# Performance work log

Measured on AMD Instinct MI355X. Metric: run time of the kernel, lower is better.

Reference implementation:

```python
import jax, jax.numpy as jnp
import numpy as np

B, T_PAST, T_FUT, GH, GW = 256, 20, 30, 100, 100
HID = 32  # past_encoder_dim


def gru_cell(x, h, w_ih, w_hh, b_ih, b_hh):
    # torch nn.GRU single-cell math; weights [3H, in], [3H, H]
    gi = x @ w_ih.T + b_ih
    gh = h @ w_hh.T + b_hh
    i_r, i_z, i_n = jnp.split(gi, 3, axis=-1)
    h_r, h_z, h_n = jnp.split(gh, 3, axis=-1)
    r = jax.nn.sigmoid(i_r + h_r)
    zg = jax.nn.sigmoid(i_z + h_z)
    n = jnp.tanh(i_n + r * h_n)
    return (1.0 - zg) * n + zg * h


def bilinear(grid, q):
    # grid [B,H,W,C]; q [B,2], dim 0 -> height, dim 1 -> width (matches torch code)
    Bn, Hh, Ww, C = grid.shape
    fy = jnp.clip(jnp.floor(q[:, 0]), 0.0, Hh - 2).astype(jnp.int32)
    fx = jnp.clip(jnp.floor(q[:, 1]), 0.0, Ww - 2).astype(jnp.int32)
    ay = jnp.clip(q[:, 0] - fy, 0.0, 1.0)[:, None]
    ax = jnp.clip(q[:, 1] - fx, 0.0, 1.0)[:, None]
    b = jnp.arange(Bn)
    tl = grid[b, fy, fx]
    tr = grid[b, fy, fx + 1]
    bl = grid[b, fy + 1, fx]
    br = grid[b, fy + 1, fx + 1]
    top = tl + ax * (tr - tl)
    bot = bl + ax * (br - bl)
    return top + ay * (bot - top)  # [B,C]


def setup_inputs() -> dict:
    key = jax.random.key(0)
    ks = jax.random.split(key, 24)
    s = 0.05
    f32 = jnp.float32
    inp = {
        'z': jax.random.normal(ks[0], (B, T_FUT, 2), f32),
        'player_past': jax.random.uniform(ks[1], (B, T_PAST, 2), f32) * (GH - 10),
        'lidar': jax.random.normal(ks[2], (B, GH, GW, 2), f32),
        'conv0_w': jax.random.normal(ks[3], (2, 2, 2, 32), f32) * s,   # HWIO
        'conv0_b': jnp.zeros((32,), f32),
        'conv1_w': jax.random.normal(ks[4], (2, 2, 32, 32), f32) * s,
        'conv1_b': jnp.zeros((32,), f32),
        'conv2_w': jax.random.normal(ks[5], (2, 2, 32, 32), f32) * s,
        'conv2_b': jnp.zeros((32,), f32),
        'conv3_w': jax.random.normal(ks[6], (2, 2, 32, 32), f32) * s,
        'conv3_b': jnp.zeros((32,), f32),
        'enc_wih': jax.random.normal(ks[7], (3 * HID, 2), f32) * s,
        'enc_whh': jax.random.normal(ks[8], (3 * HID, HID), f32) * s,
        'enc_bih': jnp.zeros((3 * HID,), f32),
        'enc_bhh': jnp.zeros((3 * HID,), f32),
        'dec_wih': jax.random.normal(ks[9], (3 * HID, HID + 2), f32) * s,
        'dec_whh': jax.random.normal(ks[10], (3 * HID, HID), f32) * s,
        'dec_bih': jnp.zeros((3 * HID,), f32),
        'dec_bhh': jnp.zeros((3 * HID,), f32),
        'mlp_w1': jax.random.normal(ks[11], (512, HID), f32) * s,
        'mlp_b1': jnp.zeros((512,), f32),
        'mlp_w2': jax.random.normal(ks[12], (4, 512), f32) * s,
        'mlp_b2': jnp.zeros((4,), f32),
    }
    return inp


def reference(z, player_past, lidar,
              conv0_w, conv0_b, conv1_w, conv1_b, conv2_w, conv2_b, conv3_w, conv3_b,
              enc_wih, enc_whh, enc_bih, enc_bhh,
              dec_wih, dec_whh, dec_bih, dec_bhh,
              mlp_w1, mlp_b1, mlp_w2, mlp_b2):
    # field model: ZeroPad2d((0,1,0,1)) + Conv 2x2 + ReLU, x4 -> same-size NHWC conv
    v = lidar
    for w, b in ((conv0_w, conv0_b), (conv1_w, conv1_b), (conv2_w, conv2_b), (conv3_w, conv3_b)):
        v = jax.nn.relu(jax.lax.conv_general_dilated(
            v, w, (1, 1), [(0, 1), (0, 1)],
            dimension_numbers=('NHWC', 'HWIO', 'NHWC')) + b)
    context_lidar = v  # [B,GH,GW,32]

    # past encoder GRU; last output of single-layer GRU == final hidden
    h0 = jnp.zeros((z.shape[0], HID), z.dtype)
    def enc_step(h, x_t):
        return gru_cell(x_t, h, enc_wih, enc_whh, enc_bih, enc_bhh), None
    h_enc, _ = jax.lax.scan(enc_step, h0, jnp.swapaxes(player_past, 0, 1))

    y_tm2 = player_past[:, -2, :]
    y_tm1 = player_past[:, -1, :]

    def dec_step(carry, z_t):
        h, y1, y2 = carry
        interp_t = bilinear(context_lidar, y1)                 # [B,32]
        x = jnp.concatenate([y1, interp_t], axis=-1)            # [B,34]
        h = gru_cell(x, h, dec_wih, dec_whh, dec_bih, dec_bhh)
        # locscale_mlp: Linear(32,512) -> Linear(512,4) (no ReLU between, per source)
        ls = (h @ mlp_w1.T + mlp_b1) @ mlp_w2.T + mlp_b2
        loc = ls[:, :2]
        scale = jax.nn.softplus(ls[:, 2:])
        y_t = 2.0 * y1 - y2 + loc + scale * z_t                 # verlet + affine sample
        return (h, y_t, y1), (y_t, scale)

    _, (ys, scales) = jax.lax.scan(dec_step, (h_enc, y_tm1, y_tm2), jnp.swapaxes(z, 0, 1))
    y = jnp.swapaxes(ys, 0, 1)          # [B,T,2]
    scales = jnp.swapaxes(scales, 0, 1)  # [B,T,2]
    logabsdet = jnp.sum(jnp.log(jnp.abs(jnp.prod(scales, axis=-2))), axis=-1)  # [B]
    return (y, logabsdet)
```

## Files before the change

kernel.cpp:

```cpp
#include <hip/hip_runtime.h>
#include <math.h>

typedef __attribute__((ext_vector_type(8))) short    short8;
typedef __attribute__((ext_vector_type(4))) float    f32x4;
typedef __attribute__((ext_vector_type(4))) unsigned uint4v;

#define FRAG0 256

__device__ __forceinline__ unsigned short f2bf(float f) {
    unsigned u = __builtin_bit_cast(unsigned, f);
    u = u + 0x7fffu + ((u >> 16) & 1u);
    return (unsigned short)(u >> 16);
}
__device__ __forceinline__ unsigned packRNE(float hi, float lo) {
    return (unsigned)f2bf(lo) | ((unsigned)f2bf(hi) << 16);
}
__device__ __forceinline__ unsigned pack_trunc(float hi, float lo) {
    return __builtin_amdgcn_perm(__builtin_bit_cast(unsigned, hi),
                                 __builtin_bit_cast(unsigned, lo), 0x07060302u);
}
__device__ __forceinline__ float rfl(float x) {
    return __builtin_bit_cast(float, __builtin_amdgcn_readfirstlane(__builtin_bit_cast(int, x)));
}
__device__ __forceinline__ f32x4 mfma16(short8 a, short8 b, f32x4 c) {
    return __builtin_amdgcn_mfma_f32_16x16x32_bf16(a, b, c, 0, 0, 0);
}
__device__ __forceinline__ unsigned bperm(int addr, unsigned v) {
    return (unsigned)__builtin_amdgcn_ds_bpermute(addr, (int)v);
}
template<int PAT>
__device__ __forceinline__ float swzXf(float v) {
    return __builtin_bit_cast(float, __builtin_amdgcn_ds_swizzle(__builtin_bit_cast(int, v), PAT));
}
__device__ __forceinline__ unsigned swz1u(unsigned v){ return (unsigned)__builtin_amdgcn_ds_swizzle((int)v, 0x041F); }
__device__ __forceinline__ float sigf(float x) { return __builtin_amdgcn_rcpf(1.f + __expf(-x)); }
__device__ __forceinline__ float tanhfast(float x) {
    float e = __expf(2.f * x);
    return 1.f - 2.f * __builtin_amdgcn_rcpf(e + 1.f);
}
__device__ __forceinline__ f32x4 ld4(const float* p) { return *(const f32x4*)p; }

__device__ __forceinline__ void packC(unsigned* P, f32x4 a0, f32x4 a1, bool oob) {
    float r0 = fmaxf(a0[0], 0.f), r1 = fmaxf(a0[1], 0.f), r2 = fmaxf(a0[2], 0.f), r3 = fmaxf(a0[3], 0.f);
    float s0 = fmaxf(a1[0], 0.f), s1 = fmaxf(a1[1], 0.f), s2 = fmaxf(a1[2], 0.f), s3 = fmaxf(a1[3], 0.f);
    P[0] = pack_trunc(r1, r0); P[1] = pack_trunc(r3, r2);
    P[2] = pack_trunc(s1, s0); P[3] = pack_trunc(s3, s2);
    if (oob) { P[0] = 0u; P[1] = 0u; P[2] = 0u; P[3] = 0u; }
}

__global__ __launch_bounds__(256) void r2p2_prep(
    const float* __restrict__ w0, const float* __restrict__ w1,
    const float* __restrict__ w2, const float* __restrict__ w3,
    const float* __restrict__ enc_whh,
    const float* __restrict__ dec_wih, const float* __restrict__ dec_whh,
    const float* __restrict__ mw1, const float* __restrict__ mb1,
    const float* __restrict__ mw2, const float* __restrict__ mb2,
    float* __restrict__ wsf, unsigned* __restrict__ wsu) {
    const int tid = threadIdx.x, bx = blockIdx.x;
    __shared__ __align__(16) short s[4224];
    __shared__ float red[64];

    if (bx == 0) {
        if (tid < 128) {
            int k = tid & 31, j = tid >> 5;
            const float* w2r = mw2 + j * 512;
            float a0 = 0.f, a1 = 0.f, a2 = 0.f, a3 = 0.f;
#pragma unroll 4
            for (int m = 0; m < 512; m += 4) {
                a0 = fmaf(w2r[m],     mw1[m * 32 + k],       a0);
                a1 = fmaf(w2r[m + 1], mw1[(m + 1) * 32 + k], a1);
                a2 = fmaf(w2r[m + 2], mw1[(m + 2) * 32 + k], a2);
                a3 = fmaf(w2r[m + 3], mw1[(m + 3) * 32 + k], a3);
            }
            wsf[j * 32 + k] = (a0 + a1) + (a2 + a3);
        } else if (tid < 192) {
            int t = tid - 128;
            int j = t & 3, ch = t >> 2;
            const float* w2c = mw2 + j * 512 + ch * 32;
            const float* b1c = mb1 + ch * 32;
            float p = 0.f;
#pragma unroll 8
            for (int m = 0; m < 32; ++m) p = fmaf(w2c[m], b1c[m], p);
            red[t] = p;
        }
        __syncthreads();
        if (tid < 4) {
            float c = mb2[tid];
#pragma unroll
            for (int i = 0; i < 16; ++i) c += red[tid + i * 4];
            wsf[128 + tid] = c;
        }
        return;
    }

    if (bx == 7) {
        if (tid < 64) {
            int lane = tid, n = lane & 15, q = lane >> 4;
            int pc0 = ((n >> 2) << 3) | (n & 3);
#pragma unroll
            for (int mt = 0; mt < 2; ++mt) {
                int co = pc0 + mt * 4;
                uint4v u = (uint4v)0u;
                if (q == 0) {
#pragma unroll
                    for (int i = 0; i < 4; ++i)
                        u[i] = packRNE(w0[(2 * i + 1) * 32 + co], w0[2 * i * 32 + co]);
                }
                *(uint4v*)(wsu + FRAG0 + mt * 256 + lane * 4) = u;
            }
        }
        return;
    }

    if (bx <= 3) {
        const float* W = (bx == 1) ? w1 : (bx == 2) ? w2 : w3;
        int fbase = 2 + (bx - 1) * 8;
        for (int i = tid; i < 4096; i += 256) {
            int k = i >> 5, co = i & 31;
            s[k * 33 + co] = (short)f2bf(W[i]);
        }
        __syncthreads();
        if (tid < 64) {
            int lane = tid, n = lane & 15, q = lane >> 4;
            int pc0 = ((n >> 2) << 3) | (n & 3);
#pragma unroll
            for (int mt = 0; mt < 2; ++mt) {
                int co = pc0 + mt * 4;
#pragma unroll
                for (int ks = 0; ks < 4; ++ks) {
                    uint4v u;
#pragma unroll
                    for (int i2 = 0; i2 < 4; ++i2) {
                        int k0 = ks * 32 + q * 8 + 2 * i2;
                        unsigned lo = (unsigned short)s[k0 * 33 + co];
                        unsigned hi = (unsigned short)s[(k0 + 1) * 33 + co];
                        u[i2] = lo | (hi << 16);
                    }
                    *(uint4v*)(wsu + FRAG0 + (fbase + mt * 4 + ks) * 256 + lane * 4) = u;
                }
            }
        }
        return;
    }

    {
        int fbase = (bx == 4) ? 26 : (bx == 5) ? 32 : 38;
        for (int i = tid; i < 3072; i += 256) {
            int o = i >> 5, k = i & 31;
            float v = (bx == 4) ? dec_wih[o * 34 + 2 + k] : (bx == 5) ? dec_whh[i] : enc_whh[i];
            s[o * 33 + k] = (short)f2bf(v);
        }
        __syncthreads();
        if (tid < 64) {
            int lane = tid, n = lane & 15, q = lane >> 4;
            int pc0 = ((n >> 2) << 3) | (n & 3);
#pragma unroll
            for (int g = 0; g < 3; ++g) {
#pragma unroll
                for (int mt = 0; mt < 2; ++mt) {
                    int row = g * 32 + pc0 + mt * 4;
                    uint4v u;
#pragma unroll
                    for (int i2 = 0; i2 < 4; ++i2) {
                        int k0 = q * 8 + 2 * i2;
                        unsigned lo = (unsigned short)s[row * 33 + k0];
                        unsigned hi = (unsigned short)s[row * 33 + k0 + 1];
                        u[i2] = lo | (hi << 16);
                    }
                    *(uint4v*)(wsu + FRAG0 + (fbase + g * 2 + mt) * 256 + lane * 4) = u;
                }
            }
        }
        return;
    }
}

__global__ __launch_bounds__(256)
void r2p2_main(
    const float* __restrict__ z, const float* __restrict__ past, const float* __restrict__ lidar,
    const float* __restrict__ b0, const float* __restrict__ b1,
    const float* __restrict__ b2, const float* __restrict__ b3,
    const float* __restrict__ enc_wih, const float* __restrict__ enc_bih, const float* __restrict__ enc_bhh,
    const float* __restrict__ dec_wih, const float* __restrict__ dec_bih, const float* __restrict__ dec_bhh,
    const float* __restrict__ wsf, const unsigned* __restrict__ wsu,
    float* __restrict__ out) {

    const int tid = threadIdx.x, b = blockIdx.x;
    const int wid = tid >> 6, lane = tid & 63;
    const int n = lane & 15, q = lane >> 4, e = n & 1;

    __shared__ __align__(16) unsigned sLID[104 * 104];
    __shared__ __align__(16) float PASTs[40];
    __shared__ __align__(16) float ZVs[64];

    if (wid != 0) {
        int st = tid - 64;
        if (st < 60) ZVs[st] = z[b * 60 + st];
        for (int i = st; i < 816; i += 192) {
            int idx = (i < 416) ? (10400 + i) : ((((i - 416) >> 2) * 104) + 100 + ((i - 416) & 3));
            sLID[idx] = 0u;
        }
        const float4* lp4 = (const float4*)(lidar + (size_t)b * 20000);
#pragma unroll 4
        for (int i = st; i < 5000; i += 192) {
            int r = (int)(((unsigned)i * 5243u) >> 18);
            int c2 = i - r * 50;
            float4 v = lp4[i];
            int o = r * 104 + 2 * c2;
            sLID[o]     = pack_trunc(v.y, v.x);
            sLID[o + 1] = pack_trunc(v.w, v.z);
        }
        __syncthreads();
        return;
    }

    uint4v FR[44];
#pragma unroll
    for (int f = 0; f < 44; ++f) FR[f] = *(const uint4v*)(wsu + FRAG0 + f * 256 + lane * 4);
#define FRG(f) __builtin_bit_cast(short8, FR[f])

    f32x4 cb0[2], cb1[2], cb2[2], cb3[2], gbR[2], gbZ[2], gbNi[2], gbNh[2];
    f32x4 egR[2], egZ[2], egNh[2];
#pragma unroll
    for (int mt = 0; mt < 2; ++mt) {
        int o = q * 8 + mt * 4;
        cb0[mt] = ld4(b0 + o); cb1[mt] = ld4(b1 + o); cb2[mt] = ld4(b2 + o); cb3[mt] = ld4(b3 + o);
        gbR[mt]  = ld4(dec_bih + o)      + ld4(dec_bhh + o);
        gbZ[mt]  = ld4(dec_bih + 32 + o) + ld4(dec_bhh + 32 + o);
        gbNi[mt] = ld4(dec_bih + 64 + o);
        gbNh[mt] = ld4(dec_bhh + 64 + o);
        egR[mt]  = ld4(enc_bih + o)      + ld4(enc_bhh + o);
        egZ[mt]  = ld4(enc_bih + 32 + o) + ld4(enc_bhh + 32 + o);
        egNh[mt] = ld4(enc_bhh + 64 + o);
    }
    f32x4 ebni = ld4(enc_bih + 64 + q * 8 + e * 4);
    float2 wxr[4], wxz[4], wxn[4], wexr[4], wexz[4], wexn[4];
#pragma unroll
    for (int r = 0; r < 4; ++r) {
        int c = q * 8 + e * 4 + r;
        wxr[r]  = *(const float2*)(dec_wih + c * 34);
        wxz[r]  = *(const float2*)(dec_wih + (32 + c) * 34);
        wxn[r]  = *(const float2*)(dec_wih + (64 + c) * 34);
        wexr[r] = *(const float2*)(enc_wih + c * 2);
        wexz[r] = *(const float2*)(enc_wih + (32 + c) * 2);
        wexn[r] = *(const float2*)(enc_wih + (64 + c) * 2);
    }
    short8 Am = (short8)0;
    if (n < 4) {
#pragma unroll
        for (int j = 0; j < 8; ++j) Am[j] = (short)f2bf(wsf[n * 32 + q * 8 + j]);
    }
    f32x4 mcv = {0.f, 0.f, 0.f, 0.f};
    if (q == 0) mcv = *(const f32x4*)(wsf + 128);

    if (lane < 20) *(float2*)&PASTs[2 * lane] = *(const float2*)(past + b * 40 + 2 * lane);
    float q0 = past[b * 40 + 38], q1 = past[b * 40 + 39];
    float p0 = past[b * 40 + 36], p1 = past[b * 40 + 37];
    asm volatile("s_waitcnt lgkmcnt(0)" ::: "memory");

    float hq[4] = {0.f, 0.f, 0.f, 0.f};
    short8 hfr = (short8)0;
#pragma unroll 1
    for (int t = 0; t < 20; ++t) {
        float2 xp = *(const float2*)&PASTs[2 * t];
        f32x4 gr0 = mfma16(FRG(38), hfr, egR[0]),  gr1 = mfma16(FRG(39), hfr, egR[1]);
        f32x4 gz0 = mfma16(FRG(40), hfr, egZ[0]),  gz1 = mfma16(FRG(41), hfr, egZ[1]);
        f32x4 gh0 = mfma16(FRG(42), hfr, egNh[0]), gh1 = mfma16(FRG(43), hfr, egNh[1]);
        f32x4 grS = e ? gr1 : gr0, gzS = e ? gz1 : gz0, ghS = e ? gh1 : gh0;
        float hn[4];
#pragma unroll
        for (int r = 0; r < 4; ++r) {
            float rp = grS[r] + xp.x * wexr[r].x + xp.y * wexr[r].y;
            float zp = gzS[r] + xp.x * wexz[r].x + xp.y * wexz[r].y;
            float pi = ebni[r] + xp.x * wexn[r].x + xp.y * wexn[r].y;
            float rr = sigf(rp), zz = sigf(zp);
            float tn = tanhfast(fmaf(rr, ghS[r], pi));
            float hv = tn + zz * (hq[r] - tn);
            hq[r] = hv; hn[r] = hv;
        }
        unsigned hu0 = packRNE(hn[1], hn[0]), hu1 = packRNE(hn[3], hn[2]);
        unsigned po0 = swz1u(hu0), po1 = swz1u(hu1);
        uint4v hv4;
        hv4[0] = e ? po0 : hu0; hv4[1] = e ? po1 : hu1;
        hv4[2] = e ? hu0 : po0; hv4[3] = e ? hu1 : po1;
        hfr = __builtin_bit_cast(short8, hv4);
    }

    __syncthreads();

    int py0a = n / 5, px0a = n % 5;
    int pe0b = (16 + n < 25) ? 16 + n : 24;
    int py0b = pe0b / 5, px0b = pe0b - py0b * 5;
    int ofs0a[4], ofs0b[4];
#pragma unroll
    for (int tp = 0; tp < 4; ++tp) {
        ofs0a[tp] = (py0a + (tp >> 1)) * 104 + px0a + (tp & 1);
        ofs0b[tp] = (py0b + (tp >> 1)) * 104 + px0b + (tp & 1);
    }
    int py1 = n >> 2, px1 = n & 3;
    int adr1[4], sel1m[4];
#pragma unroll
    for (int ks = 0; ks < 4; ++ks) {
        int p = (py1 + (ks >> 1)) * 5 + px1 + (ks & 1);
        adr1[ks] = (q * 16 + (p & 15)) * 4;
        sel1m[ks] = (p >= 16);
    }
    int pe2 = (n < 9) ? n : 8, py2 = pe2 / 3, px2 = pe2 - py2 * 3;
    int adr2[4];
#pragma unroll
    for (int ks = 0; ks < 4; ++ks) adr2[ks] = (q * 16 + (py2 + (ks >> 1)) * 4 + px2 + (ks & 1)) * 4;
    int pe3 = n & 3, py3 = pe3 >> 1, px3 = pe3 & 1;
    int adr3[4];
#pragma unroll
    for (int ks = 0; ks < 4; ++ks) adr3[ks] = (q * 16 + (py3 + (ks >> 1)) * 3 + px3 + (ks & 1)) * 4;
    const f32x4 zf4 = {0.f, 0.f, 0.f, 0.f};
    float la = 0.f;

#pragma unroll 1
    for (int t = 0; t < 30; ++t) {
        float2 zv = *(const float2*)&ZVs[2 * t];
        float f0 = fminf(fmaxf(floorf(q0), 0.f), 98.f);
        float f1v = fminf(fmaxf(floorf(q1), 0.f), 98.f);
        int fy = (int)f0, fx = (int)f1v;
        float ay = fminf(fmaxf(q0 - f0, 0.f), 1.f);
        float ax = fminf(fmaxf(q1 - f1v, 0.f), 1.f);
        int base = fy * 104 + fx;
        int limy = 100 - fy, limx = 100 - fx;

        short8 bfa = (short8)0, bfb = (short8)0;
        if (q == 0) {
            uint4v ua, ub;
#pragma unroll
            for (int tp = 0; tp < 4; ++tp) { ua[tp] = sLID[base + ofs0a[tp]]; ub[tp] = sLID[base + ofs0b[tp]]; }
            bfa = __builtin_bit_cast(short8, ua);
            bfb = __builtin_bit_cast(short8, ub);
        }
        f32x4 ca0 = mfma16(FRG(0), bfa, cb0[0]);
        f32x4 ca1 = mfma16(FRG(1), bfa, cb0[1]);
        f32x4 cB0 = mfma16(FRG(0), bfb, cb0[0]);
        f32x4 cB1 = mfma16(FRG(1), bfb, cb0[1]);
        unsigned Pa[4], Pb[4];
        packC(Pa, ca0, ca1, (py0a >= limy) || (px0a >= limx));
        packC(Pb, cB0, cB1, (py0b >= limy) || (px0b >= limx));

        short8 bf1[4];
#pragma unroll
        for (int ks = 0; ks < 4; ++ks) {
            uint4v bu;
#pragma unroll
            for (int u = 0; u < 4; ++u) {
                unsigned va = bperm(adr1[ks], Pa[u]);
                unsigned vb = bperm(adr1[ks], Pb[u]);
                bu[u] = sel1m[ks] ? vb : va;
            }
            bf1[ks] = __builtin_bit_cast(short8, bu);
        }
        {
            f32x4 aA = mfma16(FRG(2), bf1[0], cb1[0]); aA = mfma16(FRG(3), bf1[1], aA);
            f32x4 aB = mfma16(FRG(4), bf1[2], zf4);    aB = mfma16(FRG(5), bf1[3], aB);
            f32x4 bA = mfma16(FRG(6), bf1[0], cb1[1]); bA = mfma16(FRG(7), bf1[1], bA);
            f32x4 bB = mfma16(FRG(8), bf1[2], zf4);    bB = mfma16(FRG(9), bf1[3], bB);
            f32x4 o0 = aA + aB, o1 = bA + bB;
            packC(Pa, o0, o1, (py1 >= limy) || (px1 >= limx));
        }

        short8 bf2v[4];
#pragma unroll
        for (int ks = 0; ks < 4; ++ks) {
            uint4v bu;
#pragma unroll
            for (int u = 0; u < 4; ++u) bu[u] = bperm(adr2[ks], Pa[u]);
            bf2v[ks] = __builtin_bit_cast(short8, bu);
        }
        {
            f32x4 aA = mfma16(FRG(10), bf2v[0], cb2[0]); aA = mfma16(FRG(11), bf2v[1], aA);
            f32x4 aB = mfma16(FRG(12), bf2v[2], zf4);    aB = mfma16(FRG(13), bf2v[3], aB);
            f32x4 bA = mfma16(FRG(14), bf2v[0], cb2[1]); bA = mfma16(FRG(15), bf2v[1], bA);
            f32x4 bB = mfma16(FRG(16), bf2v[2], zf4);    bB = mfma16(FRG(17), bf2v[3], bB);
            f32x4 o0 = aA + aB, o1 = bA + bB;
            packC(Pb, o0, o1, (py2 >= limy) || (px2 >= limx));
        }

        short8 bf3v[4];
#pragma unroll
        for (int ks = 0; ks < 4; ++ks) {
            uint4v bu;
#pragma unroll
            for (int u = 0; u < 4; ++u) bu[u] = bperm(adr3[ks], Pb[u]);
            bf3v[ks] = __builtin_bit_cast(short8, bu);
        }
        short8 xf;
        {
            f32x4 aA = mfma16(FRG(18), bf3v[0], cb3[0]); aA = mfma16(FRG(19), bf3v[1], aA);
            f32x4 aB = mfma16(FRG(20), bf3v[2], zf4);    aB = mfma16(FRG(21), bf3v[3], aB);
            f32x4 bA = mfma16(FRG(22), bf3v[0], cb3[1]); bA = mfma16(FRG(23), bf3v[1], bA);
            f32x4 bB = mfma16(FRG(24), bf3v[2], zf4);    bB = mfma16(FRG(25), bf3v[3], bB);
            f32x4 o0 = aA + aB, o1 = bA + bB;
            float wy = (n & 2) ? ay : 1.f - ay;
            float wx = (n & 1) ? ax : 1.f - ax;
            float w = wy * wx;
            float t0[4], t1[4];
#pragma unroll
            for (int r = 0; r < 4; ++r) { t0[r] = fmaxf(o0[r], 0.f) * w; t1[r] = fmaxf(o1[r], 0.f) * w; }
#pragma unroll
            for (int r = 0; r < 4; ++r) {
                float a1 = swzXf<0x041F>(t0[r]), a2 = swzXf<0x081F>(t0[r]), a3 = swzXf<0x0C1F>(t0[r]);
                t0[r] = (t0[r] + a1) + (a2 + a3);
                float b1v = swzXf<0x041F>(t1[r]), b2v = swzXf<0x081F>(t1[r]), b3v = swzXf<0x0C1F>(t1[r]);
                t1[r] = (t1[r] + b1v) + (b2v + b3v);
            }
            uint4v xu;
            xu[0] = packRNE(t0[1], t0[0]); xu[1] = packRNE(t0[3], t0[2]);
            xu[2] = packRNE(t1[1], t1[0]); xu[3] = packRNE(t1[3], t1[2]);
            xf = __builtin_bit_cast(short8, xu);
        }

        f32x4 gr0 = mfma16(FRG(26), xf, gbR[0]); gr0 = mfma16(FRG(32), hfr, gr0);
        f32x4 gr1 = mfma16(FRG(27), xf, gbR[1]); gr1 = mfma16(FRG(33), hfr, gr1);
        f32x4 gz0 = mfma16(FRG(28), xf, gbZ[0]); gz0 = mfma16(FRG(34), hfr, gz0);
        f32x4 gz1 = mfma16(FRG(29), xf, gbZ[1]); gz1 = mfma16(FRG(35), hfr, gz1);
        f32x4 gi0 = mfma16(FRG(30), xf, gbNi[0]);
        f32x4 gi1 = mfma16(FRG(31), xf, gbNi[1]);
        f32x4 gh0 = mfma16(FRG(36), hfr, gbNh[0]);
        f32x4 gh1 = mfma16(FRG(37), hfr, gbNh[1]);
        f32x4 grS = e ? gr1 : gr0, gzS = e ? gz1 : gz0, giS = e ? gi1 : gi0, ghS = e ? gh1 : gh0;
        float hn[4];
#pragma unroll
        for (int r = 0; r < 4; ++r) {
            float rp = grS[r] + q0 * wxr[r].x + q1 * wxr[r].y;
            float zp = gzS[r] + q0 * wxz[r].x + q1 * wxz[r].y;
            float pi = giS[r] + q0 * wxn[r].x + q1 * wxn[r].y;
            float rr = sigf(rp), zz = sigf(zp);
            float tn = tanhfast(fmaf(rr, ghS[r], pi));
            float hv = tn + zz * (hq[r] - tn);
            hq[r] = hv; hn[r] = hv;
        }
        unsigned hu0 = packRNE(hn[1], hn[0]), hu1 = packRNE(hn[3], hn[2]);
        unsigned po0 = swz1u(hu0), po1 = swz1u(hu1);
        uint4v hv4;
        hv4[0] = e ? po0 : hu0; hv4[1] = e ? po1 : hu1;
        hv4[2] = e ? hu0 : po0; hv4[3] = e ? hu1 : po1;
        hfr = __builtin_bit_cast(short8, hv4);

        f32x4 ls = mfma16(Am, hfr, mcv);
        float l2 = ls[2], l3 = ls[3];
        float s0 = fmaxf(l2, 0.f) + __logf(1.f + __expf(-fabsf(l2)));
        float s1 = fmaxf(l3, 0.f) + __logf(1.f + __expf(-fabsf(l3)));
        float ny0 = 2.f * q0 - p0 + ls[0] + s0 * zv.x;
        float ny1 = 2.f * q1 - p1 + ls[1] + s1 * zv.y;
        if (lane == 0) {
            float2 o2 = {ny0, ny1};
            *(float2*)(out + b * 60 + 2 * t) = o2;
        }
        la += __logf(s0 * s1);
        p0 = q0; p1 = q1;
        q0 = rfl(ny0); q1 = rfl(ny1);
    }
    if (lane == 0) out[15360 + b] = la;
#undef FRG
}

extern "C" void kernel_launch(void* const* d_in, const int* in_sizes, int n_in,
                              void* d_out, int out_size, void* d_ws, size_t ws_size,
                              hipStream_t stream) {
    const float* z    = (const float*)d_in[0];
    const float* past = (const float*)d_in[1];
    const float* lid  = (const float*)d_in[2];
    const float* c0w = (const float*)d_in[3];  const float* c0b = (const float*)d_in[4];
    const float* c1w = (const float*)d_in[5];  const float* c1b = (const float*)d_in[6];
    const float* c2w = (const float*)d_in[7];  const float* c2b = (const float*)d_in[8];
    const float* c3w = (const float*)d_in[9];  const float* c3b = (const float*)d_in[10];
    const float* ewih = (const float*)d_in[11]; const float* ewhh = (const float*)d_in[12];
    const float* ebih = (const float*)d_in[13]; const float* ebhh = (const float*)d_in[14];
    const float* dwih = (const float*)d_in[15]; const float* dwhh = (const float*)d_in[16];
    const float* dbih = (const float*)d_in[17]; const float* dbhh = (const float*)d_in[18];
    const float* mw1 = (const float*)d_in[19]; const float* mb1 = (const float*)d_in[20];
    const float* mw2 = (const float*)d_in[21]; const float* mb2 = (const float*)d_in[22];
    float* out = (float*)d_out;
    float* wsf = (float*)d_ws;
    unsigned* wsu = (unsigned*)d_ws;

    r2p2_prep<<<8, 256, 0, stream>>>(c0w, c1w, c2w, c3w, ewhh, dwih, dwhh,
                                     mw1, mb1, mw2, mb2, wsf, wsu);
    r2p2_main<<<256, 256, 0, stream>>>(z, past, lid, c0b, c1b, c2b, c3b,
                                       ewih, ebih, ebhh, dwih, dbih, dbhh,
                                       wsf, wsu, out);
}
```

Measured before the change: 183.3 us.

## Recompute conv0 per conv1 tap to drop bperm shuffles and break MFMA chains

Conv0 is now computed directly for each of the four conv1 input taps by gathering lidar values per tap. This removes the bpermute/select shuffle that built conv1 operands from two shared conv0 tiles, at the cost of eight conv0 MFMAs instead of four and more LDS reads. The accumulation chains in conv1-3 and the GRU gates are also split into independent MFMAs summed with vector adds. That shortens dependent MFMA latency chains but adds VALU adds and register pressure.

```diff
diff --git a/kernel.cpp b/kernel.cpp
--- a/kernel.cpp
+++ b/kernel.cpp
@@ -288,22 +288,15 @@
 
     __syncthreads();
 
-    int py0a = n / 5, px0a = n % 5;
-    int pe0b = (16 + n < 25) ? 16 + n : 24;
-    int py0b = pe0b / 5, px0b = pe0b - py0b * 5;
-    int ofs0a[4], ofs0b[4];
-#pragma unroll
-    for (int tp = 0; tp < 4; ++tp) {
-        ofs0a[tp] = (py0a + (tp >> 1)) * 104 + px0a + (tp & 1);
-        ofs0b[tp] = (py0b + (tp >> 1)) * 104 + px0b + (tp & 1);
-    }
     int py1 = n >> 2, px1 = n & 3;
-    int adr1[4], sel1m[4];
+    int ofsF[4][4], pyF[4], pxF[4];
 #pragma unroll
     for (int ks = 0; ks < 4; ++ks) {
-        int p = (py1 + (ks >> 1)) * 5 + px1 + (ks & 1);
-        adr1[ks] = (q * 16 + (p & 15)) * 4;
-        sel1m[ks] = (p >= 16);
+        int pY = py1 + (ks >> 1), pX = px1 + (ks & 1);
+        pyF[ks] = pY; pxF[ks] = pX;
+#pragma unroll
+        for (int tp = 0; tp < 4; ++tp)
+            ofsF[ks][tp] = (pY + (tp >> 1)) * 104 + pX + (tp & 1);
     }
     int pe2 = (n < 9) ? n : 8, py2 = pe2 / 3, px2 = pe2 - py2 * 3;
     int adr2[4];
@@ -327,75 +320,79 @@
         int base = fy * 104 + fx;
         int limy = 100 - fy, limx = 100 - fx;
 
-        short8 bfa = (short8)0, bfb = (short8)0;
-        if (q == 0) {
-            uint4v ua, ub;
-#pragma unroll
-            for (int tp = 0; tp < 4; ++tp) { ua[tp] = sLID[base + ofs0a[tp]]; ub[tp] = sLID[base + ofs0b[tp]]; }
-            bfa = __builtin_bit_cast(short8, ua);
-            bfb = __builtin_bit_cast(short8, ub);
-        }
-        f32x4 ca0 = mfma16(FRG(0), bfa, cb0[0]);
-        f32x4 ca1 = mfma16(FRG(1), bfa, cb0[1]);
-        f32x4 cB0 = mfma16(FRG(0), bfb, cb0[0]);
-        f32x4 cB1 = mfma16(FRG(1), bfb, cb0[1]);
+        short8 bf1[4];
+#pragma unroll
+        for (int ks = 0; ks < 4; ++ks) {
+            uint4v ua = (uint4v)0u;
+            if (q == 0) {
+#pragma unroll
+                for (int tp = 0; tp < 4; ++tp) ua[tp] = sLID[base + ofsF[ks][tp]];
+            }
+            short8 bfa = __builtin_bit_cast(short8, ua);
+            f32x4 c0 = mfma16(FRG(0), bfa, cb0[0]);
+            f32x4 c1 = mfma16(FRG(1), bfa, cb0[1]);
+            uint4v P;
+            packC((unsigned*)&P, c0, c1, (pyF[ks] >= limy) || (pxF[ks] >= limx));
+            bf1[ks] = __builtin_bit_cast(short8, P);
+        }
+
         unsigned Pa[4], Pb[4];
-        packC(Pa, ca0, ca1, (py0a >= limy) || (px0a >= limx));
-        packC(Pb, cB0, cB1, (py0b >= limy) || (px0b >= limx));
-
-        short8 bf1[4];
+        {
+            f32x4 a0 = mfma16(FRG(2), bf1[0], cb1[0]);
+            f32x4 a1 = mfma16(FRG(3), bf1[1], zf4);
+            f32x4 a2 = mfma16(FRG(4), bf1[2], zf4);
+            f32x4 a3 = mfma16(FRG(5), bf1[3], zf4);
+            f32x4 b0v = mfma16(FRG(6), bf1[0], cb1[1]);
+            f32x4 b1v = mfma16(FRG(7), bf1[1], zf4);
+            f32x4 b2v = mfma16(FRG(8), bf1[2], zf4);
+            f32x4 b3v = mfma16(FRG(9), bf1[3], zf4);
+            f32x4 o0 = (a0 + a1) + (a2 + a3);
+            f32x4 o1 = (b0v + b1v) + (b2v + b3v);
+            packC(Pa, o0, o1, (py1 >= limy) || (px1 >= limx));
+        }
+
+        short8 bf2v[4];
 #pragma unroll
         for (int ks = 0; ks < 4; ++ks) {
             uint4v bu;
 #pragma unroll
-            for (int u = 0; u < 4; ++u) {
-                unsigned va = bperm(adr1[ks], Pa[u]);
-                unsigned vb = bperm(adr1[ks], Pb[u]);
-                bu[u] = sel1m[ks] ? vb : va;
-            }
-            bf1[ks] = __builtin_bit_cast(short8, bu);
+            for (int u = 0; u < 4; ++u) bu[u] = bperm(adr2[ks], Pa[u]);
+            bf2v[ks] = __builtin_bit_cast(short8, bu);
         }
         {
-            f32x4 aA = mfma16(FRG(2), bf1[0], cb1[0]); aA = mfma16(FRG(3), bf1[1], aA);
-            f32x4 aB = mfma16(FRG(4), bf1[2], zf4);    aB = mfma16(FRG(5), bf1[3], aB);
-            f32x4 bA = mfma16(FRG(6), bf1[0], cb1[1]); bA = mfma16(FRG(7), bf1[1], bA);
-            f32x4 bB = mfma16(FRG(8), bf1[2], zf4);    bB = mfma16(FRG(9), bf1[3], bB);
-            f32x4 o0 = aA + aB, o1 = bA + bB;
-            packC(Pa, o0, o1, (py1 >= limy) || (px1 >= limx));
-        }
-
-        short8 bf2v[4];
+            f32x4 a0 = mfma16(FRG(10), bf2v[0], cb2[0]);
+            f32x4 a1 = mfma16(FRG(11), bf2v[1], zf4);
+            f32x4 a2 = mfma16(FRG(12), bf2v[2], zf4);
+            f32x4 a3 = mfma16(FRG(13), bf2v[3], zf4);
+            f32x4 b0v = mfma16(FRG(14), bf2v[0], cb2[1]);
+            f32x4 b1v = mfma16(FRG(15), bf2v[1], zf4);
+            f32x4 b2v = mfma16(FRG(16), bf2v[2], zf4);
+            f32x4 b3v = mfma16(FRG(17), bf2v[3], zf4);
+            f32x4 o0 = (a0 + a1) + (a2 + a3);
+            f32x4 o1 = (b0v + b1v) + (b2v + b3v);
+            packC(Pb, o0, o1, (py2 >= limy) || (px2 >= limx));
+        }
+
+        short8 bf3v[4];
 #pragma unroll
         for (int ks = 0; ks < 4; ++ks) {
             uint4v bu;
 #pragma unroll
-            for (int u = 0; u < 4; ++u) bu[u] = bperm(adr2[ks], Pa[u]);
-            bf2v[ks] = __builtin_bit_cast(short8, bu);
-        }
-        {
-            f32x4 aA = mfma16(FRG(10), bf2v[0], cb2[0]); aA = mfma16(FRG(11), bf2v[1], aA);
-            f32x4 aB = mfma16(FRG(12), bf2v[2], zf4);    aB = mfma16(FRG(13), bf2v[3], aB);
-            f32x4 bA = mfma16(FRG(14), bf2v[0], cb2[1]); bA = mfma16(FRG(15), bf2v[1], bA);
-            f32x4 bB = mfma16(FRG(16), bf2v[2], zf4);    bB = mfma16(FRG(17), bf2v[3], bB);
-            f32x4 o0 = aA + aB, o1 = bA + bB;
-            packC(Pb, o0, o1, (py2 >= limy) || (px2 >= limx));
-        }
-
-        short8 bf3v[4];
-#pragma unroll
-        for (int ks = 0; ks < 4; ++ks) {
-            uint4v bu;
-#pragma unroll
             for (int u = 0; u < 4; ++u) bu[u] = bperm(adr3[ks], Pb[u]);
             bf3v[ks] = __builtin_bit_cast(short8, bu);
         }
         short8 xf;
         {
-            f32x4 aA = mfma16(FRG(18), bf3v[0], cb3[0]); aA = mfma16(FRG(19), bf3v[1], aA);
-            f32x4 aB = mfma16(FRG(20), bf3v[2], zf4);    aB = mfma16(FRG(21), bf3v[3], aB);
-            f32x4 bA = mfma16(FRG(22), bf3v[0], cb3[1]); bA = mfma16(FRG(23), bf3v[1], bA);
-            f32x4 bB = mfma16(FRG(24), bf3v[2], zf4);    bB = mfma16(FRG(25), bf3v[3], bB);
-            f32x4 o0 = aA + aB, o1 = bA + bB;
+            f32x4 a0 = mfma16(FRG(18), bf3v[0], cb3[0]);
+            f32x4 a1 = mfma16(FRG(19), bf3v[1], zf4);
+            f32x4 a2 = mfma16(FRG(20), bf3v[2], zf4);
+            f32x4 a3 = mfma16(FRG(21), bf3v[3], zf4);
+            f32x4 b0v = mfma16(FRG(22), bf3v[0], cb3[1]);
+            f32x4 b1v = mfma16(FRG(23), bf3v[1], zf4);
+            f32x4 b2v = mfma16(FRG(24), bf3v[2], zf4);
+            f32x4 b3v = mfma16(FRG(25), bf3v[3], zf4);
+            f32x4 o0 = (a0 + a1) + (a2 + a3);
+            f32x4 o1 = (b0v + b1v) + (b2v + b3v);
             float wy = (n & 2) ? ay : 1.f - ay;
             float wx = (n & 1) ? ax : 1.f - ax;
             float w = wy * wx;
@@ -404,10 +401,10 @@
             for (int r = 0; r < 4; ++r) { t0[r] = fmaxf(o0[r], 0.f) * w; t1[r] = fmaxf(o1[r], 0.f) * w; }
 #pragma unroll
             for (int r = 0; r < 4; ++r) {
-                float a1 = swzXf<0x041F>(t0[r]), a2 = swzXf<0x081F>(t0[r]), a3 = swzXf<0x0C1F>(t0[r]);
-                t0[r] = (t0[r] + a1) + (a2 + a3);
-                float b1v = swzXf<0x041F>(t1[r]), b2v = swzXf<0x081F>(t1[r]), b3v = swzXf<0x0C1F>(t1[r]);
-                t1[r] = (t1[r] + b1v) + (b2v + b3v);
+                float a1s = swzXf<0x041F>(t0[r]), a2s = swzXf<0x081F>(t0[r]), a3s = swzXf<0x0C1F>(t0[r]);
+                t0[r] = (t0[r] + a1s) + (a2s + a3s);
+                float b1s = swzXf<0x041F>(t1[r]), b2s = swzXf<0x081F>(t1[r]), b3s = swzXf<0x0C1F>(t1[r]);
+                t1[r] = (t1[r] + b1s) + (b2s + b3s);
             }
             uint4v xu;
             xu[0] = packRNE(t0[1], t0[0]); xu[1] = packRNE(t0[3], t0[2]);
@@ -415,10 +412,10 @@
             xf = __builtin_bit_cast(short8, xu);
         }
 
-        f32x4 gr0 = mfma16(FRG(26), xf, gbR[0]); gr0 = mfma16(FRG(32), hfr, gr0);
-        f32x4 gr1 = mfma16(FRG(27), xf, gbR[1]); gr1 = mfma16(FRG(33), hfr, gr1);
-        f32x4 gz0 = mfma16(FRG(28), xf, gbZ[0]); gz0 = mfma16(FRG(34), hfr, gz0);
-        f32x4 gz1 = mfma16(FRG(29), xf, gbZ[1]); gz1 = mfma16(FRG(35), hfr, gz1);
+        f32x4 gr0 = mfma16(FRG(26), xf, gbR[0]) + mfma16(FRG(32), hfr, zf4);
+        f32x4 gr1 = mfma16(FRG(27), xf, gbR[1]) + mfma16(FRG(33), hfr, zf4);
+        f32x4 gz0 = mfma16(FRG(28), xf, gbZ[0]) + mfma16(FRG(34), hfr, zf4);
+        f32x4 gz1 = mfma16(FRG(29), xf, gbZ[1]) + mfma16(FRG(35), hfr, zf4);
         f32x4 gi0 = mfma16(FRG(30), xf, gbNi[0]);
         f32x4 gi1 = mfma16(FRG(31), xf, gbNi[1]);
         f32x4 gh0 = mfma16(FRG(36), hfr, gbNh[0]);
```

Result: slower. 187.5 us (+2.3%).
